# Optimization experiments

Hardware: AMD Instinct MI355X
Metric: run time of the kernel (lower is better)

The kernel has to match this reference:

```python
import jax, jax.numpy as jnp
import numpy as np
import math

# Config constants (from init_kwargs)
KV_CHANNELS = 128
NUM_HEADS = 32
NUM_KV_HEADS = 2
LAYER_NUMBER = 2  # apply_query_key_layer_scaling=True -> coeff = layer_number
HEAD_DIM = KV_CHANNELS
HIDDEN = KV_CHANNELS * NUM_HEADS
COEFF = float(LAYER_NUMBER)
NORM_FACTOR = math.sqrt(HEAD_DIM) * COEFF


def setup_inputs() -> dict:
    key = jax.random.key(0)
    k1, k2, k3, k4 = jax.random.split(key, 4)
    B, Q, KV = 2, 2048, 2048
    query_layer = jax.random.normal(k1, (B, NUM_HEADS, Q, HEAD_DIM), dtype=jnp.float32)
    key_layer = jax.random.normal(k2, (B, NUM_KV_HEADS, KV, HEAD_DIM), dtype=jnp.float32)
    value_layer = jax.random.normal(k3, (B, NUM_KV_HEADS, KV, HEAD_DIM), dtype=jnp.float32)
    attention_mask = jax.random.normal(k4, (B, 1, Q, KV), dtype=jnp.float32)
    return {
        "query_layer": query_layer,
        "key_layer": key_layer,
        "value_layer": value_layer,
        "attention_mask": attention_mask,
    }


def reference(query_layer, key_layer, value_layer, attention_mask):
    # Fallback (non-FusedSDPA) path of CoreAttention.forward, eval mode (no dropout).
    b, h, q_len, d = query_layer.shape
    g = key_layer.shape[1]          # num_key_value_heads
    r = h // g                      # n_rep
    # gaudi_chatglm_repeat_kv: grouped view (b, g, r, q, d) vs kv (b, g, kv, d)
    qg = query_layer.reshape(b, g, r, q_len, d)
    # scores: (b, g, r, q, kv)
    scores = jnp.einsum("bgrqd,bgkd->bgrqk", qg, key_layer) / NORM_FACTOR
    scores = scores * COEFF
    # mask unsqueezed at dim 1 -> (b, 1, 1, q, kv), broadcast-add
    scores = scores + attention_mask[:, None]
    # softmax in fp32, cast back to query dtype
    attn = jax.nn.softmax(scores.astype(jnp.float32), axis=-1).astype(query_layer.dtype)
    # AV: (b, g, r, q, d)
    out = jnp.einsum("bgrqk,bgkd->bgrqd", attn, value_layer)
    out = out.reshape(b, h, q_len, d)
    # permute (2,0,1,3) -> (q, b, h, d); reshape -> (q, b, hidden)
    context = jnp.transpose(out, (2, 0, 1, 3)).reshape(q_len, b, h * d)
    return context
```

## Files before the change

kernel.cpp:

```cpp
#include <hip/hip_runtime.h>
#include <hip/hip_bf16.h>


constexpr int Bn = 2, Hn = 32, Gn = 2, Qn = 2048, KVn = 2048, Dn = 128;
constexpr int WAVES = 8, QBLK = 32, HO = 8;
constexpr int KVB = 64, NT = KVn / KVB;
constexpr int NT32 = KVn / 32;
constexpr float SCALE = 0.08838834764831843f;
constexpr float L2E = 1.4426950408889634f;
constexpr float SCALE2 = SCALE * L2E;

constexpr size_t WSK_BYTES = (size_t)Bn * Gn * KVn * 256;

typedef __attribute__((ext_vector_type(16))) float f32x16;
typedef __attribute__((ext_vector_type(8))) __bf16 bf16x8;
typedef __attribute__((ext_vector_type(2))) unsigned u32x2;

__device__ __forceinline__ unsigned pk2(float a, float b) {
  union { __bf16 h[2]; unsigned u; } x;
  x.h[0] = (__bf16)a; x.h[1] = (__bf16)b;
  return x.u;
}

__global__ __launch_bounds__(256)
void prepack(const float* __restrict__ Kg, const float* __restrict__ Vg,
             char* __restrict__ wsK, char* __restrict__ wsV) {
  const int i = blockIdx.x * 256 + threadIdx.x;
  {
    const int dp = i & 63, kv = (i >> 6) & (KVn - 1), bg = i >> 17;
    const float* src = Kg + ((size_t)bg * KVn + kv) * Dn + 2 * dp;
    const unsigned pr = pk2(src[0], src[1]);
    const size_t off = (size_t)bg * (KVn * 256) + (size_t)kv * 256
                       + ((4 * dp) ^ ((kv & 15) << 4));
    *(unsigned*)(wsK + off) = pr;
  }
  {
    const int d = i & 127, vg = (i >> 7) & 1023, bg = i >> 17;
    const int t = vg >> 4, vkp = vg & 15;
    const float* src = Vg + ((size_t)bg * KVn + t * 32 + 2 * vkp) * Dn + d;
    const unsigned pr = pk2(src[0], src[Dn]);
    const int slot = (((d >> 3) ^ (d >> 1)) & 3) << 4;
    const size_t off = ((size_t)bg * NT32 + t) * 8192 + (d << 6)
                       + ((vkp * 4) ^ slot);
    *(unsigned*)(wsV + off) = pr;
  }
}

__global__ __launch_bounds__(512, 2)
void attn_fwd(const float* __restrict__ Qg, const float* __restrict__ Mg,
              const char* __restrict__ wsK, const char* __restrict__ wsV,
              float* __restrict__ Og) {
  __shared__ __align__(16) short Ks[2][KVB * Dn];
  __shared__ __align__(16) short Vt[2][Dn * KVB];
  __shared__ __align__(16) float Ms[2][QBLK * KVB];

  const int tid = threadIdx.x;
  const int lane = tid & 63, w = tid >> 6;
  const int hi = lane >> 5, ln = lane & 31;
  const int qb = blockIdx.x * QBLK, ho = blockIdx.y, b = blockIdx.z;
  const int h = ho * HO + w;
  const int g = ho >> 1, bg = b * Gn + g;

  bf16x8 aq[8];
  {
    const float* qr = Qg + ((size_t)(b * Hn + h) * Qn + qb + ln) * Dn + hi * 8;
#pragma unroll
    for (int ks = 0; ks < 8; ++ks) {
      float4 f0 = *(const float4*)(qr + ks * 16);
      float4 f1 = *(const float4*)(qr + ks * 16 + 4);
      union { unsigned u[4]; bf16x8 b; } t;
      t.u[0] = pk2(f0.x * SCALE2, f0.y * SCALE2);
      t.u[1] = pk2(f0.z * SCALE2, f0.w * SCALE2);
      t.u[2] = pk2(f1.x * SCALE2, f1.y * SCALE2);
      t.u[3] = pk2(f1.z * SCALE2, f1.w * SCALE2);
      aq[ks] = t.b;
    }
  }

  const char* wsKb = wsK + (size_t)bg * (KVn * 256);
  const char* wsVb = wsV + (size_t)bg * (KVn * 256);
  const int mr = w * 4 + (lane >> 4);
  const int mc = (lane & 15) << 4;
  const char* mSrcBase = (const char*)Mg + (size_t)(b * Qn + qb + mr) * (KVn * 4)
                         + (mc ^ ((mr & 15) << 4));

  auto stage = [&](int tile, int buf) {
    const char* sk = wsKb + (size_t)tile * 16384 + w * 2048 + lane * 16;
    char* dk = (char*)Ks[buf] + w * 2048;
    __builtin_amdgcn_global_load_lds(
        (const __attribute__((address_space(1))) void*)sk,
        (__attribute__((address_space(3))) void*)dk, 16, 0, 0);
    __builtin_amdgcn_global_load_lds(
        (const __attribute__((address_space(1))) void*)(sk + 1024),
        (__attribute__((address_space(3))) void*)(dk + 1024), 16, 0, 0);
    const char* sv = wsVb + (size_t)tile * 16384 + w * 2048 + lane * 16;
    char* dv = (char*)Vt[buf] + w * 2048;
    __builtin_amdgcn_global_load_lds(
        (const __attribute__((address_space(1))) void*)sv,
        (__attribute__((address_space(3))) void*)dv, 16, 0, 0);
    __builtin_amdgcn_global_load_lds(
        (const __attribute__((address_space(1))) void*)(sv + 1024),
        (__attribute__((address_space(3))) void*)(dv + 1024), 16, 0, 0);
    const char* sm = mSrcBase + tile * 256;
    char* dm = (char*)Ms[buf] + w * 1024;
    __builtin_amdgcn_global_load_lds(
        (const __attribute__((address_space(1))) void*)sm,
        (__attribute__((address_space(3))) void*)dm, 16, 0, 0);
  };

  f32x16 o[4];
#pragma unroll
  for (int nt = 0; nt < 4; ++nt)
#pragma unroll
    for (int e = 0; e < 16; ++e) o[nt][e] = 0.0f;
  float lsum = 0.0f;

  stage(0, 0);
  __syncthreads();

  const int ksw = (ln & 15) << 4;
  const int msw = (ln & 15) << 4;

  for (int t = 0; t < NT; ++t) {
    const int cur = t & 1;
    const int tn = (t + 1 < NT) ? t + 1 : t;

    stage(tn, cur ^ 1);
    __builtin_amdgcn_sched_barrier(0);

    f32x16 s0, s1;
#pragma unroll
    for (int e = 0; e < 16; ++e) { s0[e] = 0.0f; s1[e] = 0.0f; }
    const char* ksb = (const char*)Ks[cur];
    __builtin_amdgcn_s_setprio(1);
#pragma unroll
    for (int ks = 0; ks < 8; ++ks) {
      const int byte = (ks * 32 + hi * 16) ^ ksw;
      bf16x8 k0 = *(const bf16x8*)(ksb + (ln << 8) + byte);
      bf16x8 k1 = *(const bf16x8*)(ksb + ((32 + ln) << 8) + byte);
      s0 = __builtin_amdgcn_mfma_f32_32x32x16_bf16(k0, aq[ks], s0, 0, 0, 0);
      s1 = __builtin_amdgcn_mfma_f32_32x32x16_bf16(k1, aq[ks], s1, 0, 0, 0);
    }
    __builtin_amdgcn_s_setprio(0);

    const char* msb = (const char*)Ms[cur] + ln * 256;
    unsigned own0[8], own1[8];
    float psum = 0.0f;
#pragma unroll
    for (int gq = 0; gq < 4; ++gq) {
      float4 m0 = *(const float4*)(msb + ((gq * 32 + hi * 16) ^ msw));
      float4 m1 = *(const float4*)(msb + ((128 + gq * 32 + hi * 16) ^ msw));
      float p0 = __builtin_exp2f(__builtin_fmaf(m0.x, L2E, s0[4 * gq + 0]));
      float p1 = __builtin_exp2f(__builtin_fmaf(m0.y, L2E, s0[4 * gq + 1]));
      float p2 = __builtin_exp2f(__builtin_fmaf(m0.z, L2E, s0[4 * gq + 2]));
      float p3 = __builtin_exp2f(__builtin_fmaf(m0.w, L2E, s0[4 * gq + 3]));
      float q0 = __builtin_exp2f(__builtin_fmaf(m1.x, L2E, s1[4 * gq + 0]));
      float q1 = __builtin_exp2f(__builtin_fmaf(m1.y, L2E, s1[4 * gq + 1]));
      float q2 = __builtin_exp2f(__builtin_fmaf(m1.z, L2E, s1[4 * gq + 2]));
      float q3 = __builtin_exp2f(__builtin_fmaf(m1.w, L2E, s1[4 * gq + 3]));
      psum += ((p0 + p1) + (p2 + p3)) + ((q0 + q1) + (q2 + q3));
      own0[2 * gq] = pk2(p0, p1); own0[2 * gq + 1] = pk2(p2, p3);
      own1[2 * gq] = pk2(q0, q1); own1[2 * gq + 1] = pk2(q2, q3);
    }
    lsum += psum;

    union Frag { unsigned u[4]; bf16x8 b; };
    Frag pf[4];
#pragma unroll
    for (int ks = 0; ks < 4; ++ks) {
      const unsigned* ow = (ks < 2) ? own0 : own1;
      const int bsl = (ks & 1) * 4;
#if __has_builtin(__builtin_amdgcn_permlane32_swap)
      u32x2 r0 = __builtin_amdgcn_permlane32_swap(ow[bsl + 0], ow[bsl + 2], false, false);
      u32x2 r1 = __builtin_amdgcn_permlane32_swap(ow[bsl + 1], ow[bsl + 3], false, false);
      pf[ks].u[0] = r0.x; pf[ks].u[2] = r0.y;
      pf[ks].u[1] = r1.x; pf[ks].u[3] = r1.y;
#else
      unsigned sA = __shfl_xor(ow[bsl + 0], 32), sC = __shfl_xor(ow[bsl + 2], 32);
      unsigned sB = __shfl_xor(ow[bsl + 1], 32), sD = __shfl_xor(ow[bsl + 3], 32);
      pf[ks].u[0] = hi ? sC : ow[bsl + 0];
      pf[ks].u[1] = hi ? sD : ow[bsl + 1];
      pf[ks].u[2] = hi ? ow[bsl + 2] : sA;
      pf[ks].u[3] = hi ? ow[bsl + 3] : sB;
#endif
    }

    const char* vtb = (const char*)Vt[cur];
    __builtin_amdgcn_s_setprio(1);
#pragma unroll
    for (int nt = 0; nt < 4; ++nt) {
      const int d = nt * 32 + ln;
      const int swz = (((d >> 3) ^ (d >> 1)) & 3) << 4;
#pragma unroll
      for (int ks = 0; ks < 4; ++ks) {
        const int base = (ks >> 1) * 8192 + (d << 6);
        bf16x8 vfr = *(const bf16x8*)(vtb + base + (((ks & 1) * 32 + hi * 16) ^ swz));
        o[nt] = __builtin_amdgcn_mfma_f32_32x32x16_bf16(vfr, pf[ks].b, o[nt], 0, 0, 0);
      }
    }
    __builtin_amdgcn_s_setprio(0);

    __syncthreads();
  }

  const float ltot = lsum + __shfl_xor(lsum, 32);
  const float invl = 1.0f / ltot;
  float* outp = Og + (size_t)(qb + ln) * (Bn * Hn * Dn) + (size_t)b * (Hn * Dn) + h * Dn;
#pragma unroll
  for (int nt = 0; nt < 4; ++nt)
#pragma unroll
    for (int gq = 0; gq < 4; ++gq) {
      float4 v;
      v.x = o[nt][gq * 4 + 0] * invl;
      v.y = o[nt][gq * 4 + 1] * invl;
      v.z = o[nt][gq * 4 + 2] * invl;
      v.w = o[nt][gq * 4 + 3] * invl;
      *(float4*)(outp + nt * 32 + gq * 8 + hi * 4) = v;
    }
}

extern "C" void kernel_launch(void* const* d_in, const int* in_sizes, int n_in,
                              void* d_out, int out_size, void* d_ws, size_t ws_size,
                              hipStream_t stream) {
  const float* q = (const float*)d_in[0];
  const float* k = (const float*)d_in[1];
  const float* v = (const float*)d_in[2];
  const float* m = (const float*)d_in[3];
  float* out = (float*)d_out;
  char* wsK = (char*)d_ws;
  char* wsV = wsK + WSK_BYTES;

  prepack<<<dim3((Bn * Gn * KVn * 64) / 256), 256, 0, stream>>>(k, v, wsK, wsV);
  dim3 grid(Qn / QBLK, Hn / HO, Bn);
  attn_fwd<<<grid, WAVES * 64, 0, stream>>>(q, m, wsK, wsV, out);
}
```

Before: 228.3 us.

## Software-pipeline QK of next tile with softmax/PV of current tile

Splits staging into separate K and V+mask loads, prefetching K two tiles ahead and V/mask one tile ahead. Each iteration computes the QK scores for the next tile while doing exp/softmax and PV for the current one, with score registers ping-ponging between two sets via a two-iteration unrolled loop. The intent is to overlap the MFMA work of QK with the exp-heavy softmax VALU work and hide LDS latency. The cost is more live accumulator registers, which may lower occupancy or cause spills.

```diff
diff --git a/kernel.cpp b/kernel.cpp
--- a/kernel.cpp
+++ b/kernel.cpp
@@ -84,7 +84,7 @@
   const char* mSrcBase = (const char*)Mg + (size_t)(b * Qn + qb + mr) * (KVn * 4)
                          + (mc ^ ((mr & 15) << 4));
 
-  auto stage = [&](int tile, int buf) {
+  auto stageK = [&](int tile, int buf) {
     const char* sk = wsKb + (size_t)tile * 16384 + w * 2048 + lane * 16;
     char* dk = (char*)Ks[buf] + w * 2048;
     __builtin_amdgcn_global_load_lds(
@@ -93,6 +93,8 @@
     __builtin_amdgcn_global_load_lds(
         (const __attribute__((address_space(1))) void*)(sk + 1024),
         (__attribute__((address_space(3))) void*)(dk + 1024), 16, 0, 0);
+  };
+  auto stageVM = [&](int tile, int buf) {
     const char* sv = wsVb + (size_t)tile * 16384 + w * 2048 + lane * 16;
     char* dv = (char*)Vt[buf] + w * 2048;
     __builtin_amdgcn_global_load_lds(
@@ -108,40 +110,42 @@
         (__attribute__((address_space(3))) void*)dm, 16, 0, 0);
   };
 
-  f32x16 o[4];
-#pragma unroll
-  for (int nt = 0; nt < 4; ++nt)
-#pragma unroll
-    for (int e = 0; e < 16; ++e) o[nt][e] = 0.0f;
-  float lsum = 0.0f;
-
-  stage(0, 0);
-  __syncthreads();
-
   const int ksw = (ln & 15) << 4;
   const int msw = (ln & 15) << 4;
 
-  for (int t = 0; t < NT; ++t) {
-    const int cur = t & 1;
-    const int tn = (t + 1 < NT) ? t + 1 : t;
-
-    stage(tn, cur ^ 1);
-    __builtin_amdgcn_sched_barrier(0);
-
-    f32x16 s0, s1;
-#pragma unroll
-    for (int e = 0; e < 16; ++e) { s0[e] = 0.0f; s1[e] = 0.0f; }
-    const char* ksb = (const char*)Ks[cur];
+  auto qk = [&](int buf, f32x16& t0, f32x16& t1) {
+#pragma unroll
+    for (int e = 0; e < 16; ++e) { t0[e] = 0.0f; t1[e] = 0.0f; }
+    const char* ksb = (const char*)Ks[buf];
     __builtin_amdgcn_s_setprio(1);
 #pragma unroll
     for (int ks = 0; ks < 8; ++ks) {
       const int byte = (ks * 32 + hi * 16) ^ ksw;
       bf16x8 k0 = *(const bf16x8*)(ksb + (ln << 8) + byte);
       bf16x8 k1 = *(const bf16x8*)(ksb + ((32 + ln) << 8) + byte);
-      s0 = __builtin_amdgcn_mfma_f32_32x32x16_bf16(k0, aq[ks], s0, 0, 0, 0);
-      s1 = __builtin_amdgcn_mfma_f32_32x32x16_bf16(k1, aq[ks], s1, 0, 0, 0);
+      t0 = __builtin_amdgcn_mfma_f32_32x32x16_bf16(k0, aq[ks], t0, 0, 0, 0);
+      t1 = __builtin_amdgcn_mfma_f32_32x32x16_bf16(k1, aq[ks], t1, 0, 0, 0);
     }
     __builtin_amdgcn_s_setprio(0);
+  };
+
+  f32x16 o[4];
+#pragma unroll
+  for (int nt = 0; nt < 4; ++nt)
+#pragma unroll
+    for (int e = 0; e < 16; ++e) o[nt][e] = 0.0f;
+  float lsum = 0.0f;
+
+  auto body = [&](int t, f32x16& sC0, f32x16& sC1, f32x16& sN0, f32x16& sN1) {
+    const int cur = t & 1, nxt = cur ^ 1;
+    const int tK = (t + 2 < NT) ? t + 2 : NT - 1;
+    const int tV = (t + 1 < NT) ? t + 1 : NT - 1;
+
+    stageK(tK, cur);
+    stageVM(tV, nxt);
+    __builtin_amdgcn_sched_barrier(0);
+
+    qk(nxt, sN0, sN1);
 
     const char* msb = (const char*)Ms[cur] + ln * 256;
     unsigned own0[8], own1[8];
@@ -150,14 +154,14 @@
     for (int gq = 0; gq < 4; ++gq) {
       float4 m0 = *(const float4*)(msb + ((gq * 32 + hi * 16) ^ msw));
       float4 m1 = *(const float4*)(msb + ((128 + gq * 32 + hi * 16) ^ msw));
-      float p0 = __builtin_exp2f(__builtin_fmaf(m0.x, L2E, s0[4 * gq + 0]));
-      float p1 = __builtin_exp2f(__builtin_fmaf(m0.y, L2E, s0[4 * gq + 1]));
-      float p2 = __builtin_exp2f(__builtin_fmaf(m0.z, L2E, s0[4 * gq + 2]));
-      float p3 = __builtin_exp2f(__builtin_fmaf(m0.w, L2E, s0[4 * gq + 3]));
-      float q0 = __builtin_exp2f(__builtin_fmaf(m1.x, L2E, s1[4 * gq + 0]));
-      float q1 = __builtin_exp2f(__builtin_fmaf(m1.y, L2E, s1[4 * gq + 1]));
-      float q2 = __builtin_exp2f(__builtin_fmaf(m1.z, L2E, s1[4 * gq + 2]));
-      float q3 = __builtin_exp2f(__builtin_fmaf(m1.w, L2E, s1[4 * gq + 3]));
+      float p0 = __builtin_exp2f(__builtin_fmaf(m0.x, L2E, sC0[4 * gq + 0]));
+      float p1 = __builtin_exp2f(__builtin_fmaf(m0.y, L2E, sC0[4 * gq + 1]));
+      float p2 = __builtin_exp2f(__builtin_fmaf(m0.z, L2E, sC0[4 * gq + 2]));
+      float p3 = __builtin_exp2f(__builtin_fmaf(m0.w, L2E, sC0[4 * gq + 3]));
+      float q0 = __builtin_exp2f(__builtin_fmaf(m1.x, L2E, sC1[4 * gq + 0]));
+      float q1 = __builtin_exp2f(__builtin_fmaf(m1.y, L2E, sC1[4 * gq + 1]));
+      float q2 = __builtin_exp2f(__builtin_fmaf(m1.z, L2E, sC1[4 * gq + 2]));
+      float q3 = __builtin_exp2f(__builtin_fmaf(m1.w, L2E, sC1[4 * gq + 3]));
       psum += ((p0 + p1) + (p2 + p3)) + ((q0 + q1) + (q2 + q3));
       own0[2 * gq] = pk2(p0, p1); own0[2 * gq + 1] = pk2(p2, p3);
       own1[2 * gq] = pk2(q0, q1); own1[2 * gq + 1] = pk2(q2, q3);
@@ -176,9 +180,9 @@
       pf[ks].u[0] = r0.x; pf[ks].u[2] = r0.y;
       pf[ks].u[1] = r1.x; pf[ks].u[3] = r1.y;
 #else
-      unsigned sA = __shfl_xor(ow[bsl + 0], 32), sC = __shfl_xor(ow[bsl + 2], 32);
+      unsigned sA = __shfl_xor(ow[bsl + 0], 32), sCx = __shfl_xor(ow[bsl + 2], 32);
       unsigned sB = __shfl_xor(ow[bsl + 1], 32), sD = __shfl_xor(ow[bsl + 3], 32);
-      pf[ks].u[0] = hi ? sC : ow[bsl + 0];
+      pf[ks].u[0] = hi ? sCx : ow[bsl + 0];
       pf[ks].u[1] = hi ? sD : ow[bsl + 1];
       pf[ks].u[2] = hi ? ow[bsl + 2] : sA;
       pf[ks].u[3] = hi ? ow[bsl + 3] : sB;
@@ -201,6 +205,19 @@
     __builtin_amdgcn_s_setprio(0);
 
     __syncthreads();
+  };
+
+  stageK(0, 0);
+  stageK(1, 1);
+  stageVM(0, 0);
+  __syncthreads();
+  f32x16 sA0, sA1, sB0, sB1;
+  qk(0, sA0, sA1);
+  __syncthreads();
+
+  for (int t = 0; t < NT; t += 2) {
+    body(t, sA0, sA1, sB0, sB1);
+    body(t + 1, sB0, sB1, sA0, sA1);
   }
 
   const float ltot = lsum + __shfl_xor(lsum, 32);
```

Measured after the change: 219.5 us. -3.9%, faster.
